# Kernel optimization log

Hardware: AMD Instinct MI355X
Metric: run time of the kernel (lower is better)

Reference implementation:

```python
import jax, jax.numpy as jnp
import numpy as np

N_V = 250        # n_vertices (hardcoded in module)
NUM_WS = 14
W_DIM = 512
Z_DIM = 512
B = 64
E_PER = 1488     # ~directed convex-hull edges per graph (3N-6 undirected)
LR = 0.01        # lr_multiplier
CAM_R = 1.3


def _fc(x, w, b):
    # StyleGAN FullyConnectedLayer: runtime weight gain lr/sqrt(fan_in), bias gain lr,
    # bias_act 'lrelu' (alpha=0.2) with gain sqrt(2).
    gain = LR / np.sqrt(w.shape[1])
    y = x @ (w.T * gain) + b * LR
    return jax.nn.leaky_relu(y, 0.2) * np.sqrt(2.0)


def _seg_mean(vals, idx, n):
    s = jax.ops.segment_sum(vals, idx, num_segments=n)
    c = jax.ops.segment_sum(jnp.ones((idx.shape[0], 1), vals.dtype), idx, num_segments=n)
    return s / jnp.maximum(c, 1.0)


def _processor(x, edge_index, edge_attr, ew0, eb0, ew1, eb1, nw0, nb0, nw1, nb1, out_dim):
    src, dst = edge_index[0], edge_index[1]
    # edge encoder on [x_recv, x_send, edge_attr]
    ef = jnp.concatenate([x[src], x[dst], edge_attr], axis=-1)
    ef = _fc(_fc(ef, ew0, eb0), ew1, eb1)
    # PyG propagate (flow source_to_target): message = cat([x_i, edge_attr]) with
    # x_i = x[edge_index[1]], mean-aggregated onto edge_index[1].
    msg = jnp.concatenate([x[dst], ef], axis=-1)
    agg = _seg_mean(msg, dst, x.shape[0])
    nf = jnp.concatenate([x, agg[:, out_dim:]], axis=-1)
    nf = _fc(_fc(nf, nw0, nb0), nw1, nb1)
    return nf, ef


def setup_inputs() -> dict:
    key = jax.random.key(0)
    ks = jax.random.split(key, 24)
    z = jax.random.normal(ks[0], (B, Z_DIM), jnp.float32)
    la = jax.random.normal(ks[1], (B * N_V, 3), jnp.float32)
    look_ats = -CAM_R * la / jnp.linalg.norm(la, axis=-1, keepdims=True)
    # block-structured edges: each graph's edges stay within its 250-node block
    rng = np.random.default_rng(0)
    base = np.repeat(np.arange(B, dtype=np.int32) * N_V, E_PER)
    src = base + rng.integers(0, N_V, size=B * E_PER).astype(np.int32)
    dst = base + rng.integers(0, N_V, size=B * E_PER).astype(np.int32)
    edge_index = jnp.asarray(np.stack([src, dst]))
    # FullyConnectedLayer weights: init N(0,1)/lr_multiplier, bias 0
    def w(k, o, i):
        return jax.random.normal(k, (o, i), jnp.float32) / LR
    D = W_DIM
    inp = dict(z=z, look_ats=look_ats, edge_index=edge_index)
    inp.update(
        p0_ew0=w(ks[2], D, 1034), p0_eb0=jnp.zeros((D,), jnp.float32),
        p0_ew1=w(ks[3], D, D),    p0_eb1=jnp.zeros((D,), jnp.float32),
        p0_nw0=w(ks[4], D, 1030), p0_nb0=jnp.zeros((D,), jnp.float32),
        p0_nw1=w(ks[5], D, D),    p0_nb1=jnp.zeros((D,), jnp.float32),
        p1_ew0=w(ks[6], D, 1536), p1_eb0=jnp.zeros((D,), jnp.float32),
        p1_ew1=w(ks[7], D, D),    p1_eb1=jnp.zeros((D,), jnp.float32),
        p1_nw0=w(ks[8], D, 1024), p1_nb0=jnp.zeros((D,), jnp.float32),
        p1_nw1=w(ks[9], D, D),    p1_nb1=jnp.zeros((D,), jnp.float32),
    )
    return inp


def reference(z, look_ats, edge_index,
              p0_ew0, p0_eb0, p0_ew1, p0_eb1, p0_nw0, p0_nb0, p0_nw1, p0_nb1,
              p1_ew0, p1_eb0, p1_ew1, p1_eb1, p1_nw0, p1_nb0, p1_nw1, p1_nb1):
    b = z.shape[0]
    # normalize_2nd_moment
    zn = z * jax.lax.rsqrt(jnp.mean(jnp.square(z), axis=-1, keepdims=True) + 1e-8)
    # generate_graph: x = cat([z.repeat(N,1), look_ats]); edge_attr from look_ats
    x = jnp.concatenate([jnp.tile(zn, (N_V, 1)), look_ats], axis=-1)  # [B*N, 515]
    rel = look_ats[edge_index[1]] - look_ats[edge_index[0]]
    dist = jnp.linalg.norm(rel, axis=-1, keepdims=True)
    ea = jnp.concatenate([rel, dist], axis=-1)  # [E, 4]
    x, ea = _processor(x, edge_index, ea, p0_ew0, p0_eb0, p0_ew1, p0_eb1,
                       p0_nw0, p0_nb0, p0_nw1, p0_nb1, W_DIM)
    x, ea = _processor(x, edge_index, ea, p1_ew0, p1_eb0, p1_ew1, p1_eb1,
                       p1_nw0, p1_nb0, p1_nw1, p1_nb1, W_DIM)
    ws = x[::N_V]                        # in_ids = [i*N for i in range(B)]
    return jnp.tile(ws[:, None, :], (1, NUM_WS, 1))  # [B, num_ws, w_dim]
```

## Files before the change

kernel.cpp:

```cpp
#include <hip/hip_runtime.h>
#include <hip/hip_bf16.h>
#include <cmath>

#define NVP 250
#define NN  16000
#define EN  95232
#define LRc 0.01f
#define SQ2 1.41421356237309515f

#define CAP_ES 1024
#define CAP_N1 1024
#define CAP_E0 4096
#define EBLK ((EN + 255) / 256)
#define NBLK ((NN + 255) / 256)
#define SK_T 4

typedef __attribute__((ext_vector_type(8))) short bf16x8;
typedef __attribute__((ext_vector_type(4))) float f32x4;

__device__ __forceinline__ unsigned short bfc(float x) {
  unsigned u = __builtin_bit_cast(unsigned, x);
  u = (u + 0x7fffu + ((u >> 16) & 1u)) >> 16;
  return (unsigned short)u;
}
__device__ __forceinline__ unsigned pk2(float a, float b) {
  return (unsigned)bfc(a) | ((unsigned)bfc(b) << 16);
}

struct GMX {
  const float* W; const float* Ain; float* pbuf; const int* Mdev;
  const float* cnt; const int* listN1;
  int Wld, Woff, Astride, K, KC, Mcap, Mfix;
};

template<int VECW, int SCALED>
__global__ __launch_bounds__(256) void gemmM2(GMX p) {
  int M = p.Mdev ? *p.Mdev : p.Mfix;
  if (M > p.Mcap) M = p.Mcap;
  const int mBase = blockIdx.x * 64;
  if (mBase >= M) return;
  const int nBase = blockIdx.y * 64;
  const int z = blockIdx.z;
  int kBeg = z * p.KC, kEnd = kBeg + p.KC;
  if (kEnd > p.K) kEnd = p.K;

  __shared__ unsigned short Abf[64*72];
  __shared__ unsigned short Wbf[64*72];
  const int t = threadIdx.x;
  const int srow = t >> 2, sq = (t & 3) * 16;
  int arow = mBase + srow; if (arow >= M) arow = M - 1;
  float s = 1.f;
  if (SCALED) s = 1.0f / fmaxf(p.cnt[p.listN1[arow]], 1.0f);
  const float* aRow = p.Ain + (size_t)arow * p.Astride + sq;
  const float* wRow = p.W + (size_t)(nBase + srow) * p.Wld + p.Woff + sq;

  float4 ra[4], rw[4];
  auto ld = [&](int kt) {
#pragma unroll
    for (int i = 0; i < 4; i++) {
      ra[i] = *(const float4*)(aRow + kt + 4*i);
      if (VECW) {
        rw[i] = *(const float4*)(wRow + kt + 4*i);
      } else {
        const float* wp = wRow + kt + 4*i;
        rw[i] = make_float4(wp[0], wp[1], wp[2], wp[3]);
      }
    }
  };
  ld(kBeg);

  const int lane = t & 63, wv = t >> 6;
  const int fr = wv*16 + (lane & 15);
  const int fcol = (lane & 15);
  const int fo = (lane >> 4) * 8;
  f32x4 acc0 = {}, acc1 = {}, acc2 = {}, acc3 = {};

  for (int kt = kBeg; kt < kEnd; kt += 64) {
    if (kt > kBeg) __syncthreads();
    unsigned short* da = &Abf[srow*72 + sq];
    unsigned short* dw = &Wbf[srow*72 + sq];
#pragma unroll
    for (int i = 0; i < 4; i++) {
      uint2 ua; ua.x = pk2(ra[i].x*s, ra[i].y*s); ua.y = pk2(ra[i].z*s, ra[i].w*s);
      *(uint2*)&da[i*4] = ua;
      uint2 uw; uw.x = pk2(rw[i].x, rw[i].y); uw.y = pk2(rw[i].z, rw[i].w);
      *(uint2*)&dw[i*4] = uw;
    }
    __syncthreads();
    if (kt + 64 < kEnd) ld(kt + 64);
#pragma unroll
    for (int kk = 0; kk < 64; kk += 32) {
      bf16x8 a = *(const bf16x8*)&Abf[fr*72 + kk + fo];
      bf16x8 b0 = *(const bf16x8*)&Wbf[( 0 + fcol)*72 + kk + fo];
      bf16x8 b1 = *(const bf16x8*)&Wbf[(16 + fcol)*72 + kk + fo];
      bf16x8 b2 = *(const bf16x8*)&Wbf[(32 + fcol)*72 + kk + fo];
      bf16x8 b3 = *(const bf16x8*)&Wbf[(48 + fcol)*72 + kk + fo];
      acc0 = __builtin_amdgcn_mfma_f32_16x16x32_bf16(a, b0, acc0, 0, 0, 0);
      acc1 = __builtin_amdgcn_mfma_f32_16x16x32_bf16(a, b1, acc1, 0, 0, 0);
      acc2 = __builtin_amdgcn_mfma_f32_16x16x32_bf16(a, b2, acc2, 0, 0, 0);
      acc3 = __builtin_amdgcn_mfma_f32_16x16x32_bf16(a, b3, acc3, 0, 0, 0);
    }
  }
  float* ob = p.pbuf + (size_t)z * p.Mcap * 512;
  int orow = mBase + wv*16 + (lane >> 4) * 4;
  int oc = nBase + fcol;
#pragma unroll
  for (int r = 0; r < 4; r++) {
    float* q = ob + (size_t)(orow + r) * 512 + oc;
    q[0] = acc0[r]; q[16] = acc1[r]; q[32] = acc2[r]; q[48] = acc3[r];
  }
}

struct GMG {
  const float* W; const float* x1c; const float* ef0c;
  const int* listES; const int* src; const int* dst; const int* posN; const int* posOf;
  const int* Mdev; float* pbuf; int KC;
};
__global__ __launch_bounds__(256) void gemmGM2(GMG p) {
  int M = *p.Mdev; if (M > CAP_ES) M = CAP_ES;
  const int mBase = blockIdx.x * 64;
  if (mBase >= M) return;
  const int nBase = blockIdx.y * 64;
  const int z = blockIdx.z;
  int kBeg = z * p.KC, kEnd = kBeg + p.KC;

  __shared__ unsigned short Abf[64*72];
  __shared__ unsigned short Wbf[64*72];
  const int t = threadIdx.x;
  const int srow = t >> 2, sq = (t & 3) * 16;
  int arow = mBase + srow; if (arow >= M) arow = M - 1;
  int e = p.listES[arow];
  const float* s0 = p.x1c + (size_t)p.posN[p.src[e]] * 512;
  const float* s1 = p.x1c + (size_t)p.posN[p.dst[e]] * 512;
  const float* s2 = p.ef0c + (size_t)p.posOf[e] * 512;
  const float* wRow = p.W + (size_t)(nBase + srow) * 1536 + sq;

  float4 ra[4], rw[4];
  auto ld = [&](int kt) {
    int ka = kt + sq;
    const float* ap = (ka < 512) ? (s0 + ka) : (ka < 1024) ? (s1 + ka - 512)
                                                           : (s2 + ka - 1024);
#pragma unroll
    for (int i = 0; i < 4; i++) {
      ra[i] = *(const float4*)(ap + 4*i);
      rw[i] = *(const float4*)(wRow + kt + 4*i);
    }
  };
  ld(kBeg);

  const int lane = t & 63, wv = t >> 6;
  const int fr = wv*16 + (lane & 15);
  const int fcol = (lane & 15);
  const int fo = (lane >> 4) * 8;
  f32x4 acc0 = {}, acc1 = {}, acc2 = {}, acc3 = {};

  for (int kt = kBeg; kt < kEnd; kt += 64) {
    if (kt > kBeg) __syncthreads();
    unsigned short* da = &Abf[srow*72 + sq];
    unsigned short* dw = &Wbf[srow*72 + sq];
#pragma unroll
    for (int i = 0; i < 4; i++) {
      uint2 ua; ua.x = pk2(ra[i].x, ra[i].y); ua.y = pk2(ra[i].z, ra[i].w);
      *(uint2*)&da[i*4] = ua;
      uint2 uw; uw.x = pk2(rw[i].x, rw[i].y); uw.y = pk2(rw[i].z, rw[i].w);
      *(uint2*)&dw[i*4] = uw;
    }
    __syncthreads();
    if (kt + 64 < kEnd) ld(kt + 64);
#pragma unroll
    for (int kk = 0; kk < 64; kk += 32) {
      bf16x8 a = *(const bf16x8*)&Abf[fr*72 + kk + fo];
      bf16x8 b0 = *(const bf16x8*)&Wbf[( 0 + fcol)*72 + kk + fo];
      bf16x8 b1 = *(const bf16x8*)&Wbf[(16 + fcol)*72 + kk + fo];
      bf16x8 b2 = *(const bf16x8*)&Wbf[(32 + fcol)*72 + kk + fo];
      bf16x8 b3 = *(const bf16x8*)&Wbf[(48 + fcol)*72 + kk + fo];
      acc0 = __builtin_amdgcn_mfma_f32_16x16x32_bf16(a, b0, acc0, 0, 0, 0);
      acc1 = __builtin_amdgcn_mfma_f32_16x16x32_bf16(a, b1, acc1, 0, 0, 0);
      acc2 = __builtin_amdgcn_mfma_f32_16x16x32_bf16(a, b2, acc2, 0, 0, 0);
      acc3 = __builtin_amdgcn_mfma_f32_16x16x32_bf16(a, b3, acc3, 0, 0, 0);
    }
  }
  float* ob = p.pbuf + (size_t)z * CAP_ES * 512;
  int orow = mBase + wv*16 + (lane >> 4) * 4;
  int oc = nBase + fcol;
#pragma unroll
  for (int r = 0; r < 4; r++) {
    float* q = ob + (size_t)(orow + r) * 512 + oc;
    q[0] = acc0[r]; q[16] = acc1[r]; q[32] = acc2[r]; q[48] = acc3[r];
  }
}

template<int VECW, int NSEG>
__device__ __forceinline__ void gemm_loop(
    const float* const* b0, const float* const* b1,
    const float* sc0, const float* sc1,
    const float* w0, const float* w1, const float* w2, const float* w3,
    int kBeg, int kEnd,
    float (*As)[36], float (*Bs)[68], float acc[4][4]) {
  const int t = threadIdx.x;
  const int k4 = (t & 7) * 4;
  const int mr = t >> 3;
  const int tx = t & 15, ty = t >> 4;
  float4 ra0, ra1, rw0, rw1, rw2, rw3;
  auto lA = [&](int k0) {
// ... 33 lines not shown
    if (k0 + 32 < kEnd) { lA(k0 + 32); lW(k0 + 32); }
#pragma unroll
    for (int kk = 0; kk < 32; kk++) {
      float4 a4 = *(const float4*)&As[kk][ty*4];
      float4 b4 = *(const float4*)&Bs[kk][tx*4];
      float aa[4] = {a4.x, a4.y, a4.z, a4.w};
      float bb[4] = {b4.x, b4.y, b4.z, b4.w};
#pragma unroll
      for (int i = 0; i < 4; i++)
#pragma unroll
        for (int j = 0; j < 4; j++) acc[i][j] += aa[i]*bb[j];
    }
  }
}

struct GPP {
  const float* W; const float* Ain; float* pbuf; const int* Mdev;
  const float* cnt; const int* listN1;
  int Wld, Woff, Astride, K, KC, Mcap, Mfix;
};
template<int VECW, int SCALED>
__global__ __launch_bounds__(128) void gemmP(GPP p) {
  int M = p.Mdev ? *p.Mdev : p.Mfix;
  if (M > p.Mcap) M = p.Mcap;
  const int mBase = blockIdx.x * 32;
  if (mBase >= M) return;
  const int nBase = blockIdx.y * 64;
  const int z = blockIdx.z;
  int kBeg = z * p.KC;
  int kEnd = kBeg + p.KC; if (kEnd > p.K) kEnd = p.K;
  __shared__ float As[32][36];
  __shared__ float Bs[32][68];
  const int t = threadIdx.x;
  const float* b0[1]; const float* b1[1]; float sc0[1] = {1.f}, sc1[1] = {1.f};
  int rA = mBase + (t >> 3);
  b0[0] = p.Ain + (size_t)rA * p.Astride;
  b1[0] = b0[0] + (size_t)16 * p.Astride;
  if (SCALED) {
    int ra = rA < M ? rA : M-1;
    int rb = (rA+16) < M ? rA+16 : M-1;
    sc0[0] = 1.0f / fmaxf(p.cnt[p.listN1[ra]], 1.0f);
    sc1[0] = 1.0f / fmaxf(p.cnt[p.listN1[rb]], 1.0f);
  }
  const int kofs = (t & 7)*4 + p.Woff;
  const float* w0 = p.W + (size_t)(nBase + (t>>3)) * p.Wld + kofs;
  const float* w1 = w0 + (size_t)16 * p.Wld;
  const float* w2 = w0 + (size_t)32 * p.Wld;
  const float* w3 = w0 + (size_t)48 * p.Wld;
  float acc[4][4] = {};
  gemm_loop<VECW, 1>(b0, b1, sc0, sc1, w0, w1, w2, w3, kBeg, kEnd, As, Bs, acc);
  const int tx = t & 15, ty = t >> 4;
#pragma unroll
  for (int i = 0; i < 4; i++) {
    int r = mBase + ty*4 + i;
    *(float4*)&p.pbuf[((size_t)z*p.Mcap + r)*512 + nBase + tx*4] =
      make_float4(acc[i][0],acc[i][1],acc[i][2],acc[i][3]);
  }
}

struct GTP {
  const float* W; const float* x1c; const float* agg1c; const float* cnt;
  const int* posN; float* pbuf; int KC;
};
__global__ __launch_bounds__(128) void gemmT(GTP p) {
  const int mBase = blockIdx.x * 32;
  const int nBase = blockIdx.y * 64;
  const int z = blockIdx.z;
  int kBeg = z * p.KC, kEnd = kBeg + p.KC;
  __shared__ float As[32][36];
  __shared__ float Bs[32][68];
  const int t = threadIdx.x;
  int r0 = mBase + (t>>3), r1 = r0 + 16;
  const float* b0[2] = { p.x1c + (size_t)p.posN[r0*NVP]*512,
                         p.agg1c + (size_t)r0*512 - 512 };
  const float* b1[2] = { p.x1c + (size_t)p.posN[r1*NVP]*512,
                         p.agg1c + (size_t)r1*512 - 512 };
  float sc0[2] = {1.f, 1.0f / fmaxf(p.cnt[r0*NVP], 1.0f)};
  float sc1[2] = {1.f, 1.0f / fmaxf(p.cnt[r1*NVP], 1.0f)};
  const int kofs = (t & 7)*4;
  const float* w0 = p.W + (size_t)(nBase + (t>>3)) * 1024 + kofs;
  const float* w1 = w0 + (size_t)16 * 1024;
  const float* w2 = w0 + (size_t)32 * 1024;
  const float* w3 = w0 + (size_t)48 * 1024;
  float acc[4][4] = {};
  gemm_loop<1, 2>(b0, b1, sc0, sc1, w0, w1, w2, w3, kBeg, kEnd, As, Bs, acc);
  const int tx = t & 15, ty = t >> 4;
#pragma unroll
  for (int i = 0; i < 4; i++) {
    int r = mBase + ty*4 + i;
    *(float4*)&p.pbuf[((size_t)z*64 + r)*512 + nBase + tx*4] =
      make_float4(acc[i][0],acc[i][1],acc[i][2],acc[i][3]);
  }
}

struct TABP { const float* zn; const float* We; const float* Wn;
              float* pbTs; float* pbTd; float* pbT0; };
__global__ __launch_bounds__(128) void tab_k(TABP q) {
  int wsel = blockIdx.y >> 3;
  int nBase = (blockIdx.y & 7) * 64;
  const float* W = (wsel == 2) ? q.Wn : q.We;
  int Wld = (wsel == 2) ? 1030 : 1034;
  int Woff = (wsel == 1) ? 515 : 0;
  float* pb = (wsel == 0) ? q.pbTs : (wsel == 1) ? q.pbTd : q.pbT0;
  int z = blockIdx.z;
  __shared__ float As[32][36];
  __shared__ float Bs[32][68];
// ... 6 lines not shown
  const float* w0 = W + (size_t)(nBase + (t>>3)) * Wld + kofs;
  const float* w1 = w0 + (size_t)16 * Wld;
  const float* w2 = w0 + (size_t)32 * Wld;
  const float* w3 = w0 + (size_t)48 * Wld;
  float acc[4][4] = {};
  gemm_loop<0, 1>(b0, b1, sc0, sc1, w0, w1, w2, w3, z*128, z*128+128, As, Bs, acc);
  const int tx = t & 15, ty = t >> 4;
#pragma unroll
  for (int i = 0; i < 4; i++) {
    int r = mBase + ty*4 + i;
    *(float4*)&pb[((size_t)z*64 + r)*512 + nBase + tx*4] =
      make_float4(acc[i][0],acc[i][1],acc[i][2],acc[i][3]);
  }
}

struct EPP {
  const float* pbuf; const float* bias; const float* T0p; const float* la;
  const float* cnt; const float* w0n;
  const int* rmap; const int* dst; const int* posN; const int* Mdev;
  float* outp; float* atomp;
  int SK, Mcap, Mfix; float gain;
};

template<int EPI>
__global__ __launch_bounds__(256) void epi_k(EPP e) {
  int M = e.Mdev ? *e.Mdev : e.Mfix;
  if (M > e.Mcap) M = e.Mcap;
  int i = blockIdx.x*256 + threadIdx.x;
  if (i >= M*128) return;
  int m = i >> 7, n4 = (i & 127) * 4;
  float ys[4] = {0.f, 0.f, 0.f, 0.f};
  for (int z = 0; z < e.SK; z++) {
    float4 v = *(const float4*)&e.pbuf[((size_t)z*e.Mcap + m)*512 + n4];
    ys[0] += v.x; ys[1] += v.y; ys[2] += v.z; ys[3] += v.w;
  }
  if (EPI == 7) {
    int nd = e.rmap[m];
    int rr = nd & 63;
#pragma unroll
    for (int z = 0; z < SK_T; z++) {
      float4 v = *(const float4*)&e.T0p[((size_t)z*64 + rr)*512 + n4];
      ys[0] += v.x; ys[1] += v.y; ys[2] += v.z; ys[3] += v.w;
    }
    float l0 = e.la[nd*3], l1 = e.la[nd*3+1], l2 = e.la[nd*3+2];
    bool has = e.cnt[nd] > 0.f;
#pragma unroll
    for (int j = 0; j < 4; j++) {
      int n = n4 + j;
      float corr = l0*e.w0n[0*512+n] + l1*e.w0n[1*512+n] + l2*e.w0n[2*512+n];
      if (has) corr += l0*e.w0n[3*512+n] + l1*e.w0n[4*512+n] + l2*e.w0n[5*512+n];
      ys[j] += corr;
    }
  }
#pragma unroll
  for (int j = 0; j < 4; j++) {
    float y = ys[j] * e.gain + e.bias[n4+j] * LRc;
    ys[j] = (y > 0.f ? y : 0.2f*y) * SQ2;
  }
  float4 ov = make_float4(ys[0], ys[1], ys[2], ys[3]);
  if (EPI == 0 || EPI == 7) {
    *(float4*)&e.outp[(size_t)m*512 + n4] = ov;
  } else if (EPI == 1) {
    *(float4*)&e.outp[(size_t)m*512 + n4] = ov;
    int tr = e.posN[e.dst[e.rmap[m]]];
#pragma unroll
    for (int j = 0; j < 4; j++) atomicAdd(&e.atomp[(size_t)tr*512 + n4 + j], ys[j]);
  } else if (EPI == 2) {
    int tr = e.dst[e.rmap[m]] / NVP;
#pragma unroll
    for (int j = 0; j < 4; j++) atomicAdd(&e.atomp[(size_t)tr*512 + n4 + j], ys[j]);
  } else {
#pragma unroll
    for (int w = 0; w < 14; w++)
      *(float4*)&e.outp[((size_t)(m*14 + w))*512 + n4] = ov;
  }
}

__global__ __launch_bounds__(256) void init_k(const float* z, float* zn, int* need,
                                              const float* W0, const float* Wn,
                                              float* w0s, float* w0n) {
  int b = blockIdx.x, t = threadIdx.x;
  if (b < 64) {
    float s = 0.f;
    for (int j = t; j < 512; j += 256) { float v = z[b*512+j]; s += v*v; }
    for (int o = 32; o > 0; o >>= 1) s += __shfl_down(s, o);
    __shared__ float red[5];
    if ((t & 63) == 0) red[t >> 6] = s;
    __syncthreads();
    if (t == 0) {
      float tot = red[0]+red[1]+red[2]+red[3];
      red[4] = 1.0f / sqrtf(tot * (1.0f/512.0f) + 1e-8f);
    }
// ... 20 lines not shown
  unsigned long long m = __ballot(pred);
  int lane = threadIdx.x & 63, w = threadIdx.x >> 6;
  if (lane == 0) ws4[w] = __popcll(m);
  __syncthreads();
  return ws4[0] + ws4[1] + ws4[2] + ws4[3];
}
__device__ __forceinline__ int blockRank(int pred, int* ws4) {
  unsigned long long m = __ballot(pred);
  int lane = threadIdx.x & 63, w = threadIdx.x >> 6;
  if (lane == 0) ws4[w] = __popcll(m);
  __syncthreads();
  int off = 0;
  for (int i = 0; i < w; i++) off += ws4[i];
  return off + __popcll(m & ((1ull << lane) - 1ull));
}

__global__ __launch_bounds__(256) void cntES_k(const int* src, const int* dst,
                                               float* cnt, int* need, int* bcnt) {
  __shared__ int ws4[4];
  int e = blockIdx.x*256 + threadIdx.x;
  int pred = 0;
  if (e < EN) {
    int d = dst[e];
    atomicAdd(&cnt[d], 1.0f);
    pred = (d % NVP) == 0;
    if (pred) need[src[e]] = 1;
  }
  int c = blockCount(pred, ws4);
  if (threadIdx.x == 0) bcnt[blockIdx.x] = c;
}
// ... 1 lines not shown
                                                 int* bcntE, int* bcntN) {
  __shared__ int ws4[4];
  int b = blockIdx.x;
  if (b < EBLK) {
    int e = b*256 + threadIdx.x;
    int pred = (e < EN) && need[dst[e]];
    int c = blockCount(pred, ws4);
    if (threadIdx.x == 0) bcntE[b] = c;
  } else {
    int n = (b-EBLK)*256 + threadIdx.x;
    int pred = (n < NN) && need[n];
    int c = blockCount(pred, ws4);
    if (threadIdx.x == 0) bcntN[b-EBLK] = c;
  }
}
__global__ __launch_bounds__(512) void scan3_k(const int* bA, int nA, int* oA, int* tA,
                                               const int* bB, int nB, int* oB, int* tB,
                                               const int* bC, int nC, int* oC, int* tC) {
  const int* bcnt; int n; int* boff; int* tot;
  if (blockIdx.x == 0)      { bcnt = bA; n = nA; boff = oA; tot = tA; }
  else if (blockIdx.x == 1) { bcnt = bB; n = nB; boff = oB; tot = tB; }
  else                      { bcnt = bC; n = nC; boff = oC; tot = tC; }
  __shared__ int s[512];
  int t = threadIdx.x;
  int orig = (t < n) ? bcnt[t] : 0;
  s[t] = orig;
  __syncthreads();
  for (int o = 1; o < 512; o <<= 1) {
    int v = (t >= o) ? s[t-o] : 0;
    __syncthreads();
    s[t] += v;
    __syncthreads();
  }
  if (t < n) boff[t] = s[t] - orig;
  if (t == n-1) *tot = s[t];
}
__global__ __launch_bounds__(256) void emit3_k(const int* src, const int* dst,
                                               const int* need,
                                               const int* boffS, int* listES,
                                               const int* boffE, int* listE0, int* posOf,
                                               const int* boffN, int* listN1, int* posN) {
  __shared__ int ws4[4];
  int b = blockIdx.x;
  if (b < EBLK) {
    int e = b*256 + threadIdx.x;
    int pred = (e < EN) && (dst[e] % NVP == 0);
    int rank = blockRank(pred, ws4);
    if (pred) {
      int pos = boffS[b] + rank;
      if (pos < CAP_ES) listES[pos] = e;
    }
  } else if (b < 2*EBLK) {
    int e = (b-EBLK)*256 + threadIdx.x;
    int pred = (e < EN) && need[dst[e]];
    int rank = blockRank(pred, ws4);
    if (pred) {
      int pos = boffE[b-EBLK] + rank;
      if (pos < CAP_E0) { listE0[pos] = e; posOf[e] = pos; }
    }
  } else {
    int n = (b-2*EBLK)*256 + threadIdx.x;
    int pred = (n < NN) && need[n];
    int rank = blockRank(pred, ws4);
    if (pred) {
      int pos = boffN[b-2*EBLK] + rank;
      if (pos < CAP_N1) { listN1[pos] = n; posN[n] = pos; }
    }
  }
}

__global__ __launch_bounds__(128) void edge0_k(const int* nE0p, const int* listE0,
                                               const int* src, const int* dst,
                                               const float* pbTs, const float* pbTd,
                                               const float* la, const float* w0s,
                                               const float* b0, float* h0c) {
  int i = blockIdx.x;
  int n0 = *nE0p; if (n0 > CAP_E0) n0 = CAP_E0;
  if (i >= n0) return;
  int tid = threadIdx.x;
  int e = listE0[i];
  int s = src[e], d = dst[e];
  float a0 = la[s*3], a1 = la[s*3+1], a2 = la[s*3+2];
// ... 47 lines not shown
  const float* p1eb1 = (const float*)d_in[14];
  const float* p1nw0 = (const float*)d_in[15];
  const float* p1nb0 = (const float*)d_in[16];
  const float* p1nw1 = (const float*)d_in[17];
  const float* p1nb1 = (const float*)d_in[18];
  const int* src = ei;
  const int* dst = ei + EN;

  char* ws = (char*)d_ws;
  size_t off = 0;
  auto al = [&](size_t bytes) -> void* {
    void* r = (void*)(ws + off);
    off += (bytes + 255) & ~(size_t)255;
    return r;
  };
  int*   tot    = (int*)  al(3*4);
  float* cnt    = (float*)al(NN*4);
  int*   need   = (int*)  al(NN*4);
  int*   posN   = (int*)  al(NN*4);
  int*   posOf  = (int*)  al((size_t)EN*4);
  int*   bcntS  = (int*)  al(EBLK*4);
  int*   boffS  = (int*)  al(EBLK*4);
  int*   bcntE  = (int*)  al(EBLK*4);
  int*   boffE  = (int*)  al(EBLK*4);
  int*   bcntN  = (int*)  al(NBLK*4);
  int*   boffN  = (int*)  al(NBLK*4);
  int*   listES = (int*)  al(CAP_ES*4);
  int*   listN1 = (int*)  al(CAP_N1*4);
  int*   listE0 = (int*)  al(CAP_E0*4);
  float* agg0c  = (float*)al((size_t)CAP_N1*512*4);
  float* agg1c  = (float*)al(64*512*4);
  size_t zEnd = off;
  float* zn     = (float*)al(64*512*4);
  float* w0s    = (float*)al(10*512*4);
  float* w0n    = (float*)al(6*512*4);
  float* pbTs   = (float*)al((size_t)SK_T*64*512*4);
  float* pbTd   = (float*)al((size_t)SK_T*64*512*4);
  float* pbT0   = (float*)al((size_t)SK_T*64*512*4);
  float* h0c    = (float*)al((size_t)CAP_E0*512*4);
  float* ef0c   = (float*)al((size_t)CAP_E0*512*4);
  float* hn1    = (float*)al((size_t)CAP_N1*512*4);
  float* x1c    = (float*)al((size_t)CAP_N1*512*4);
  float* hs     = (float*)al((size_t)CAP_ES*512*4);
  float* hn64   = (float*)al(64*512*4);
  float* pbuf   = (float*)al((size_t)16384*512*4);

  hipMemsetAsync(ws, 0, zEnd, stream);

  init_k<<<129, 256, 0, stream>>>(z, zn, need, p0ew0, p0nw0, w0s, w0n);
  cntES_k<<<EBLK, 256, 0, stream>>>(src, dst, cnt, need, bcntS);
  cntE0N1_k<<<EBLK+NBLK, 256, 0, stream>>>(dst, need, bcntE, bcntN);
  scan3_k<<<3, 512, 0, stream>>>(bcntS, EBLK, boffS, tot+0,
                                 bcntE, EBLK, boffE, tot+1,
                                 bcntN, NBLK, boffN, tot+2);
  emit3_k<<<2*EBLK+NBLK, 256, 0, stream>>>(src, dst, need, boffS, listES,
                                           boffE, listE0, posOf, boffN, listN1, posN);
  {
    TABP q{zn, p0ew0, p0nw0, pbTs, pbTd, pbT0};
    tab_k<<<dim3(2, 24, SK_T), 128, 0, stream>>>(q);
  }
  edge0_k<<<CAP_E0, 128, 0, stream>>>(tot+1, listE0, src, dst, pbTs, pbTd, la, w0s,
                                      p0eb0, h0c);

  {
    GMX p{}; p.W = p0ew1; p.Wld = 512; p.Woff = 0; p.Astride = 512;
    p.K = 512; p.KC = 256; p.Mcap = CAP_E0; p.Mdev = tot+1; p.Ain = h0c; p.pbuf = pbuf;
    gemmM2<1,0><<<dim3(CAP_E0/64, 8, 2), 256, 0, stream>>>(p);
    EPP e{}; e.pbuf = pbuf; e.SK = 2; e.Mcap = CAP_E0; e.Mdev = tot+1;
    e.bias = p0eb1; e.gain = LRc/sqrtf(512.f);
    e.rmap = listE0; e.dst = dst; e.posN = posN; e.outp = ef0c; e.atomp = agg0c;
    epi_k<1><<<(CAP_E0*128)/256, 256, 0, stream>>>(e);
  }
  {
    GMX p{}; p.W = p0nw0; p.Wld = 1030; p.Woff = 518; p.Astride = 512;
    p.K = 512; p.KC = 128; p.Mcap = CAP_N1; p.Mdev = tot+2;
    p.Ain = agg0c; p.cnt = cnt; p.listN1 = listN1; p.pbuf = pbuf;
    gemmM2<0,1><<<dim3(CAP_N1/64, 8, 4), 256, 0, stream>>>(p);
    EPP e{}; e.pbuf = pbuf; e.SK = 4; e.Mcap = CAP_N1; e.Mdev = tot+2;
    e.bias = p0nb0; e.gain = LRc/sqrtf(1030.f);
    e.T0p = pbT0; e.rmap = listN1; e.la = la; e.cnt = cnt; e.w0n = w0n; e.outp = hn1;
    epi_k<7><<<(CAP_N1*128)/256, 256, 0, stream>>>(e);
  }
  {
    GMX p{}; p.W = p0nw1; p.Wld = 512; p.Woff = 0; p.Astride = 512;
    p.K = 512; p.KC = 128; p.Mcap = CAP_N1; p.Mdev = tot+2; p.Ain = hn1; p.pbuf = pbuf;
    gemmM2<1,0><<<dim3(CAP_N1/64, 8, 4), 256, 0, stream>>>(p);
    EPP e{}; e.pbuf = pbuf; e.SK = 4; e.Mcap = CAP_N1; e.Mdev = tot+2;
    e.bias = p0nb1; e.gain = LRc/sqrtf(512.f); e.outp = x1c;
    epi_k<0><<<(CAP_N1*128)/256, 256, 0, stream>>>(e);
  }
  {
    GMG p{}; p.W = p1ew0; p.x1c = x1c; p.ef0c = ef0c;
    p.listES = listES; p.src = src; p.dst = dst; p.posN = posN; p.posOf = posOf;
    p.Mdev = tot+0; p.pbuf = pbuf; p.KC = 256;
    gemmGM2<<<dim3(CAP_ES/64, 8, 6), 256, 0, stream>>>(p);
    EPP e{}; e.pbuf = pbuf; e.SK = 6; e.Mcap = CAP_ES; e.Mdev = tot+0;
    e.bias = p1eb0; e.gain = LRc/sqrtf(1536.f); e.outp = hs;
    epi_k<0><<<(CAP_ES*128)/256, 256, 0, stream>>>(e);
  }
  {
    GMX p{}; p.W = p1ew1; p.Wld = 512; p.Woff = 0; p.Astride = 512;
    p.K = 512; p.KC = 128; p.Mcap = CAP_ES; p.Mdev = tot+0; p.Ain = hs; p.pbuf = pbuf;
    gemmM2<1,0><<<dim3(CAP_ES/64, 8, 4), 256, 0, stream>>>(p);
    EPP e{}; e.pbuf = pbuf; e.SK = 4; e.Mcap = CAP_ES; e.Mdev = tot+0;
    e.bias = p1eb1; e.gain = LRc/sqrtf(512.f);
    e.rmap = listES; e.dst = dst; e.atomp = agg1c;
    epi_k<2><<<(CAP_ES*128)/256, 256, 0, stream>>>(e);
  }
  {
    GTP p{}; p.W = p1nw0; p.x1c = x1c; p.agg1c = agg1c; p.cnt = cnt;
    p.posN = posN; p.pbuf = pbuf; p.KC = 128;
    gemmT<<<dim3(2, 8, 8), 128, 0, stream>>>(p);
    EPP e{}; e.pbuf = pbuf; e.SK = 8; e.Mcap = 64; e.Mfix = 64;
    e.bias = p1nb0; e.gain = LRc/sqrtf(1024.f); e.outp = hn64;
    epi_k<0><<<(64*128)/256, 256, 0, stream>>>(e);
  }
  {
    GPP p{}; p.W = p1nw1; p.Wld = 512; p.Woff = 0; p.Astride = 512;
    p.K = 512; p.KC = 128; p.Mcap = 64; p.Mfix = 64; p.Mdev = nullptr;
    p.Ain = hn64; p.pbuf = pbuf;
    gemmP<1,0><<<dim3(2, 8, 4), 128, 0, stream>>>(p);
    EPP e{}; e.pbuf = pbuf; e.SK = 4; e.Mcap = 64; e.Mfix = 64;
    e.bias = p1nb1; e.gain = LRc/sqrtf(512.f); e.outp = (float*)d_out;
    epi_k<8><<<(64*128)/256, 256, 0, stream>>>(e);
  }
}
```

Before: 145.5 us.

## Fuse GEMM epilogues into kernels, drop split-K, merge scan into emit

Removes split-K partial buffers and the separate epilogue kernels. Each GEMM now runs the full K loop and applies bias, leaky-relu, row remapping and scatter atomics straight from the MFMA accumulators. The scan kernel is also folded into the emit kernel, where each block recomputes its prefix by summing the block counts. This cuts about seven kernel launches and the partial-sum traffic, but each kernel now has fewer blocks with longer K loops, and epilogue stores and atomics become less coalesced.

```diff
diff --git a/kernel.cpp b/kernel.cpp
--- a/kernel.cpp
+++ b/kernel.cpp
@@ -27,22 +27,85 @@
   return (unsigned)bfc(a) | ((unsigned)bfc(b) << 16);
 }
 
-struct GMX {
-  const float* W; const float* Ain; float* pbuf; const int* Mdev;
+struct FEP {
+  const float* bias; float gain;
+  const float* T0p; const float* la; const float* cnt; const float* w0n;
+  const int* rmap; const int* dst; const int* posN;
+  float* outp; float* atomp;
+};
+
+template<int EPI>
+__device__ __forceinline__ void mfma_epi(const FEP& f, f32x4 acc0, f32x4 acc1,
+                                         f32x4 acc2, f32x4 acc3,
+                                         int mBase, int nBase, int M,
+                                         int lane, int wv) {
+  const int fcol = lane & 15;
+  int rows[4]; bool rok[4]; int tr[4];
+  int rr4[4]; float la0[4], la1[4], la2[4]; bool has[4];
+#pragma unroll
+  for (int r = 0; r < 4; r++) {
+    int row = mBase + wv*16 + (lane >> 4)*4 + r;
+    rows[r] = row; rok[r] = row < M;
+    int rc = rok[r] ? row : 0;
+    if (EPI == 1) tr[r] = f.posN[f.dst[f.rmap[rc]]];
+    if (EPI == 2) tr[r] = f.dst[f.rmap[rc]] / NVP;
+    if (EPI == 7) {
+      int nd = f.rmap[rc];
+      rr4[r] = nd & 63;
+      la0[r] = f.la[nd*3]; la1[r] = f.la[nd*3+1]; la2[r] = f.la[nd*3+2];
+      has[r] = f.cnt[nd] > 0.f;
+    }
+  }
+  f32x4 accs[4] = {acc0, acc1, acc2, acc3};
+#pragma unroll
+  for (int c = 0; c < 4; c++) {
+    int n = nBase + fcol + 16*c;
+    float bi = f.bias[n] * LRc;
+    float w6[6];
+    if (EPI == 7) {
+#pragma unroll
+      for (int j = 0; j < 6; j++) w6[j] = f.w0n[j*512 + n];
+    }
+#pragma unroll
+    for (int r = 0; r < 4; r++) {
+      if (!rok[r]) continue;
+      float yr = accs[c][r];
+      if (EPI == 7) {
+#pragma unroll
+        for (int zz = 0; zz < SK_T; zz++)
+          yr += f.T0p[((size_t)zz*64 + rr4[r])*512 + n];
+        float corr = la0[r]*w6[0] + la1[r]*w6[1] + la2[r]*w6[2];
+        if (has[r]) corr += la0[r]*w6[3] + la1[r]*w6[4] + la2[r]*w6[5];
+        yr += corr;
+      }
+      float y = yr * f.gain + bi;
+      y = (y > 0.f ? y : 0.2f*y) * SQ2;
+      if (EPI == 0 || EPI == 7) {
+        f.outp[(size_t)rows[r]*512 + n] = y;
+      } else if (EPI == 1) {
+        f.outp[(size_t)rows[r]*512 + n] = y;
+        atomicAdd(&f.atomp[(size_t)tr[r]*512 + n], y);
+      } else {
+        atomicAdd(&f.atomp[(size_t)tr[r]*512 + n], y);
+      }
+    }
+  }
+}
+
+struct GMF {
+  const float* W; const float* Ain; const int* Mdev;
   const float* cnt; const int* listN1;
-  int Wld, Woff, Astride, K, KC, Mcap, Mfix;
+  int Wld, Woff, Astride, K, Mcap, Mfix;
+  FEP f;
 };
 
-template<int VECW, int SCALED>
-__global__ __launch_bounds__(256) void gemmM2(GMX p) {
+template<int VECW, int SCALED, int EPI>
+__global__ __launch_bounds__(256) void gemmMF(GMF p) {
   int M = p.Mdev ? *p.Mdev : p.Mfix;
   if (M > p.Mcap) M = p.Mcap;
   const int mBase = blockIdx.x * 64;
   if (mBase >= M) return;
   const int nBase = blockIdx.y * 64;
-  const int z = blockIdx.z;
-  int kBeg = z * p.KC, kEnd = kBeg + p.KC;
-  if (kEnd > p.K) kEnd = p.K;
 
   __shared__ unsigned short Abf[64*72];
   __shared__ unsigned short Wbf[64*72];
@@ -67,7 +130,7 @@
       }
     }
   };
-  ld(kBeg);
+  ld(0);
 
   const int lane = t & 63, wv = t >> 6;
   const int fr = wv*16 + (lane & 15);
@@ -75,8 +138,8 @@
   const int fo = (lane >> 4) * 8;
   f32x4 acc0 = {}, acc1 = {}, acc2 = {}, acc3 = {};
 
-  for (int kt = kBeg; kt < kEnd; kt += 64) {
-    if (kt > kBeg) __syncthreads();
+  for (int kt = 0; kt < p.K; kt += 64) {
+    if (kt > 0) __syncthreads();
     unsigned short* da = &Abf[srow*72 + sq];
     unsigned short* dw = &Wbf[srow*72 + sq];
 #pragma unroll
@@ -87,7 +150,7 @@
       *(uint2*)&dw[i*4] = uw;
     }
     __syncthreads();
-    if (kt + 64 < kEnd) ld(kt + 64);
+    if (kt + 64 < p.K) ld(kt + 64);
 #pragma unroll
     for (int kk = 0; kk < 64; kk += 32) {
       bf16x8 a = *(const bf16x8*)&Abf[fr*72 + kk + fo];
@@ -101,28 +164,20 @@
       acc3 = __builtin_amdgcn_mfma_f32_16x16x32_bf16(a, b3, acc3, 0, 0, 0);
     }
   }
-  float* ob = p.pbuf + (size_t)z * p.Mcap * 512;
-  int orow = mBase + wv*16 + (lane >> 4) * 4;
-  int oc = nBase + fcol;
-#pragma unroll
-  for (int r = 0; r < 4; r++) {
-    float* q = ob + (size_t)(orow + r) * 512 + oc;
-    q[0] = acc0[r]; q[16] = acc1[r]; q[32] = acc2[r]; q[48] = acc3[r];
-  }
-}
-
-struct GMG {
+  mfma_epi<EPI>(p.f, acc0, acc1, acc2, acc3, mBase, nBase, M, lane, wv);
+}
+
+struct GGF {
   const float* W; const float* x1c; const float* ef0c;
   const int* listES; const int* src; const int* dst; const int* posN; const int* posOf;
-  const int* Mdev; float* pbuf; int KC;
+  const int* Mdev;
+  FEP f;
 };
-__global__ __launch_bounds__(256) void gemmGM2(GMG p) {
+__global__ __launch_bounds__(256) void gemmGF(GGF p) {
   int M = *p.Mdev; if (M > CAP_ES) M = CAP_ES;
   const int mBase = blockIdx.x * 64;
   if (mBase >= M) return;
   const int nBase = blockIdx.y * 64;
-  const int z = blockIdx.z;
-  int kBeg = z * p.KC, kEnd = kBeg + p.KC;
 
   __shared__ unsigned short Abf[64*72];
   __shared__ unsigned short Wbf[64*72];
@@ -146,7 +201,7 @@
       rw[i] = *(const float4*)(wRow + kt + 4*i);
     }
   };
-  ld(kBeg);
+  ld(0);
 
   const int lane = t & 63, wv = t >> 6;
   const int fr = wv*16 + (lane & 15);
@@ -154,8 +209,8 @@
   const int fo = (lane >> 4) * 8;
   f32x4 acc0 = {}, acc1 = {}, acc2 = {}, acc3 = {};
 
-  for (int kt = kBeg; kt < kEnd; kt += 64) {
-    if (kt > kBeg) __syncthreads();
+  for (int kt = 0; kt < 1536; kt += 64) {
+    if (kt > 0) __syncthreads();
     unsigned short* da = &Abf[srow*72 + sq];
     unsigned short* dw = &Wbf[srow*72 + sq];
 #pragma unroll
@@ -166,7 +221,7 @@
       *(uint2*)&dw[i*4] = uw;
     }
     __syncthreads();
-    if (kt + 64 < kEnd) ld(kt + 64);
+    if (kt + 64 < 1536) ld(kt + 64);
 #pragma unroll
     for (int kk = 0; kk < 64; kk += 32) {
       bf16x8 a = *(const bf16x8*)&Abf[fr*72 + kk + fo];
@@ -180,14 +235,7 @@
       acc3 = __builtin_amdgcn_mfma_f32_16x16x32_bf16(a, b3, acc3, 0, 0, 0);
     }
   }
-  float* ob = p.pbuf + (size_t)z * CAP_ES * 512;
-  int orow = mBase + wv*16 + (lane >> 4) * 4;
-  int oc = nBase + fcol;
-#pragma unroll
-  for (int r = 0; r < 4; r++) {
-    float* q = ob + (size_t)(orow + r) * 512 + oc;
-    q[0] = acc0[r]; q[16] = acc1[r]; q[32] = acc2[r]; q[48] = acc3[r];
-  }
+  mfma_epi<0>(p.f, acc0, acc1, acc2, acc3, mBase, nBase, M, lane, wv);
 }
 
 template<int VECW, int NSEG>
@@ -251,59 +299,14 @@
   }
 }
 
-struct GPP {
-  const float* W; const float* Ain; float* pbuf; const int* Mdev;
-  const float* cnt; const int* listN1;
-  int Wld, Woff, Astride, K, KC, Mcap, Mfix;
+struct GTF {
+  const float* W; const float* x1c; const float* agg1c; const float* cnt;
+  const int* posN;
+  const float* bias; float gain; float* outp;
 };
-template<int VECW, int SCALED>
-__global__ __launch_bounds__(128) void gemmP(GPP p) {
-  int M = p.Mdev ? *p.Mdev : p.Mfix;
-  if (M > p.Mcap) M = p.Mcap;
-  const int mBase = blockIdx.x * 32;
-  if (mBase >= M) return;
-  const int nBase = blockIdx.y * 64;
-  const int z = blockIdx.z;
-  int kBeg = z * p.KC;
-  int kEnd = kBeg + p.KC; if (kEnd > p.K) kEnd = p.K;
-  __shared__ float As[32][36];
-  __shared__ float Bs[32][68];
-  const int t = threadIdx.x;
-  const float* b0[1]; const float* b1[1]; float sc0[1] = {1.f}, sc1[1] = {1.f};
-  int rA = mBase + (t >> 3);
-  b0[0] = p.Ain + (size_t)rA * p.Astride;
-  b1[0] = b0[0] + (size_t)16 * p.Astride;
-  if (SCALED) {
-    int ra = rA < M ? rA : M-1;
-    int rb = (rA+16) < M ? rA+16 : M-1;
-    sc0[0] = 1.0f / fmaxf(p.cnt[p.listN1[ra]], 1.0f);
-    sc1[0] = 1.0f / fmaxf(p.cnt[p.listN1[rb]], 1.0f);
-  }
-  const int kofs = (t & 7)*4 + p.Woff;
-  const float* w0 = p.W + (size_t)(nBase + (t>>3)) * p.Wld + kofs;
-  const float* w1 = w0 + (size_t)16 * p.Wld;
-  const float* w2 = w0 + (size_t)32 * p.Wld;
-  const float* w3 = w0 + (size_t)48 * p.Wld;
-  float acc[4][4] = {};
-  gemm_loop<VECW, 1>(b0, b1, sc0, sc1, w0, w1, w2, w3, kBeg, kEnd, As, Bs, acc);
-  const int tx = t & 15, ty = t >> 4;
-#pragma unroll
-  for (int i = 0; i < 4; i++) {
-    int r = mBase + ty*4 + i;
-    *(float4*)&p.pbuf[((size_t)z*p.Mcap + r)*512 + nBase + tx*4] =
-      make_float4(acc[i][0],acc[i][1],acc[i][2],acc[i][3]);
-  }
-}
-
-struct GTP {
-  const float* W; const float* x1c; const float* agg1c; const float* cnt;
-  const int* posN; float* pbuf; int KC;
-};
-__global__ __launch_bounds__(128) void gemmT(GTP p) {
+__global__ __launch_bounds__(128) void gemmTF(GTF p) {
   const int mBase = blockIdx.x * 32;
   const int nBase = blockIdx.y * 64;
-  const int z = blockIdx.z;
-  int kBeg = z * p.KC, kEnd = kBeg + p.KC;
   __shared__ float As[32][36];
   __shared__ float Bs[32][68];
   const int t = threadIdx.x;
@@ -320,13 +323,60 @@
   const float* w2 = w0 + (size_t)32 * 1024;
   const float* w3 = w0 + (size_t)48 * 1024;
   float acc[4][4] = {};
-  gemm_loop<1, 2>(b0, b1, sc0, sc1, w0, w1, w2, w3, kBeg, kEnd, As, Bs, acc);
+  gemm_loop<1, 2>(b0, b1, sc0, sc1, w0, w1, w2, w3, 0, 1024, As, Bs, acc);
   const int tx = t & 15, ty = t >> 4;
+  float4 bv = *(const float4*)&p.bias[nBase + tx*4];
+  float bb[4] = {bv.x, bv.y, bv.z, bv.w};
 #pragma unroll
   for (int i = 0; i < 4; i++) {
     int r = mBase + ty*4 + i;
-    *(float4*)&p.pbuf[((size_t)z*64 + r)*512 + nBase + tx*4] =
-      make_float4(acc[i][0],acc[i][1],acc[i][2],acc[i][3]);
+    float ys[4];
+#pragma unroll
+    for (int j = 0; j < 4; j++) {
+      float y = acc[i][j] * p.gain + bb[j] * LRc;
+      ys[j] = (y > 0.f ? y : 0.2f*y) * SQ2;
+    }
+    *(float4*)&p.outp[(size_t)r*512 + nBase + tx*4] =
+      make_float4(ys[0], ys[1], ys[2], ys[3]);
+  }
+}
+
+struct GPF2 {
+  const float* W; const float* Ain;
+  const float* bias; float gain; float* outp;
+};
+__global__ __launch_bounds__(128) void gemmPF(GPF2 p) {
+  const int mBase = blockIdx.x * 32;
+  const int nBase = blockIdx.y * 64;
+  __shared__ float As[32][36];
+  __shared__ float Bs[32][68];
+  const int t = threadIdx.x;
+  const float* b0[1]; const float* b1[1]; float sc0[1] = {1.f}, sc1[1] = {1.f};
+  b0[0] = p.Ain + (size_t)(mBase + (t>>3)) * 512;
+  b1[0] = b0[0] + (size_t)16 * 512;
+  const int kofs = (t & 7)*4;
+  const float* w0 = p.W + (size_t)(nBase + (t>>3)) * 512 + kofs;
+  const float* w1 = w0 + (size_t)16 * 512;
+  const float* w2 = w0 + (size_t)32 * 512;
+  const float* w3 = w0 + (size_t)48 * 512;
+  float acc[4][4] = {};
+  gemm_loop<1, 1>(b0, b1, sc0, sc1, w0, w1, w2, w3, 0, 512, As, Bs, acc);
+  const int tx = t & 15, ty = t >> 4;
+  float4 bv = *(const float4*)&p.bias[nBase + tx*4];
+  float bb[4] = {bv.x, bv.y, bv.z, bv.w};
+#pragma unroll
+  for (int i = 0; i < 4; i++) {
+    int r = mBase + ty*4 + i;
+    float ys[4];
+#pragma unroll
+    for (int j = 0; j < 4; j++) {
+      float y = acc[i][j] * p.gain + bb[j] * LRc;
+      ys[j] = (y > 0.f ? y : 0.2f*y) * SQ2;
+    }
+    float4 ov = make_float4(ys[0], ys[1], ys[2], ys[3]);
+#pragma unroll
+    for (int w = 0; w < 14; w++)
+      *(float4*)&p.outp[((size_t)(r*14 + w))*512 + nBase + tx*4] = ov;
   }
 }
 
@@ -363,68 +413,6 @@
   }
 }
 
-struct EPP {
-  const float* pbuf; const float* bias; const float* T0p; const float* la;
-  const float* cnt; const float* w0n;
-  const int* rmap; const int* dst; const int* posN; const int* Mdev;
-  float* outp; float* atomp;
-  int SK, Mcap, Mfix; float gain;
-};
-
-template<int EPI>
-__global__ __launch_bounds__(256) void epi_k(EPP e) {
-  int M = e.Mdev ? *e.Mdev : e.Mfix;
-  if (M > e.Mcap) M = e.Mcap;
-  int i = blockIdx.x*256 + threadIdx.x;
-  if (i >= M*128) return;
-  int m = i >> 7, n4 = (i & 127) * 4;
-  float ys[4] = {0.f, 0.f, 0.f, 0.f};
-  for (int z = 0; z < e.SK; z++) {
-    float4 v = *(const float4*)&e.pbuf[((size_t)z*e.Mcap + m)*512 + n4];
-    ys[0] += v.x; ys[1] += v.y; ys[2] += v.z; ys[3] += v.w;
-  }
-  if (EPI == 7) {
-    int nd = e.rmap[m];
-    int rr = nd & 63;
-#pragma unroll
-    for (int z = 0; z < SK_T; z++) {
-      float4 v = *(const float4*)&e.T0p[((size_t)z*64 + rr)*512 + n4];
-      ys[0] += v.x; ys[1] += v.y; ys[2] += v.z; ys[3] += v.w;
-    }
-    float l0 = e.la[nd*3], l1 = e.la[nd*3+1], l2 = e.la[nd*3+2];
-    bool has = e.cnt[nd] > 0.f;
-#pragma unroll
-    for (int j = 0; j < 4; j++) {
-      int n = n4 + j;
-      float corr = l0*e.w0n[0*512+n] + l1*e.w0n[1*512+n] + l2*e.w0n[2*512+n];
-      if (has) corr += l0*e.w0n[3*512+n] + l1*e.w0n[4*512+n] + l2*e.w0n[5*512+n];
-      ys[j] += corr;
-    }
-  }
-#pragma unroll
-  for (int j = 0; j < 4; j++) {
-    float y = ys[j] * e.gain + e.bias[n4+j] * LRc;
-    ys[j] = (y > 0.f ? y : 0.2f*y) * SQ2;
-  }
-  float4 ov = make_float4(ys[0], ys[1], ys[2], ys[3]);
-  if (EPI == 0 || EPI == 7) {
-    *(float4*)&e.outp[(size_t)m*512 + n4] = ov;
-  } else if (EPI == 1) {
-    *(float4*)&e.outp[(size_t)m*512 + n4] = ov;
-    int tr = e.posN[e.dst[e.rmap[m]]];
-#pragma unroll
-    for (int j = 0; j < 4; j++) atomicAdd(&e.atomp[(size_t)tr*512 + n4 + j], ys[j]);
-  } else if (EPI == 2) {
-    int tr = e.dst[e.rmap[m]] / NVP;
-#pragma unroll
-    for (int j = 0; j < 4; j++) atomicAdd(&e.atomp[(size_t)tr*512 + n4 + j], ys[j]);
-  } else {
-#pragma unroll
-    for (int w = 0; w < 14; w++)
-      *(float4*)&e.outp[((size_t)(m*14 + w))*512 + n4] = ov;
-  }
-}
-
 __global__ __launch_bounds__(256) void init_k(const float* z, float* zn, int* need,
                                               const float* W0, const float* Wn,
                                               float* w0s, float* w0n) {
@@ -475,6 +463,16 @@
   for (int i = 0; i < w; i++) off += ws4[i];
   return off + __popcll(m & ((1ull << lane) - 1ull));
 }
+__device__ __forceinline__ int blockSumN(const int* arr, int n, int* red) {
+  int local = 0;
+  for (int i = threadIdx.x; i < n; i += 256) local += arr[i];
+  for (int o = 32; o > 0; o >>= 1) local += __shfl_down(local, o);
+  if ((threadIdx.x & 63) == 0) red[threadIdx.x >> 6] = local;
+  __syncthreads();
+  int s = red[0]+red[1]+red[2]+red[3];
+  __syncthreads();
+  return s;
+}
 
 __global__ __launch_bounds__(256) void cntES_k(const int* src, const int* dst,
                                                float* cnt, int* need, int* bcnt) {
@@ -506,58 +504,41 @@
     if (threadIdx.x == 0) bcntN[b-EBLK] = c;
   }
 }
-__global__ __launch_bounds__(512) void scan3_k(const int* bA, int nA, int* oA, int* tA,
-                                               const int* bB, int nB, int* oB, int* tB,
-                                               const int* bC, int nC, int* oC, int* tC) {
-  const int* bcnt; int n; int* boff; int* tot;
-  if (blockIdx.x == 0)      { bcnt = bA; n = nA; boff = oA; tot = tA; }
-  else if (blockIdx.x == 1) { bcnt = bB; n = nB; boff = oB; tot = tB; }
-  else                      { bcnt = bC; n = nC; boff = oC; tot = tC; }
-  __shared__ int s[512];
-  int t = threadIdx.x;
-  int orig = (t < n) ? bcnt[t] : 0;
-  s[t] = orig;
-  __syncthreads();
-  for (int o = 1; o < 512; o <<= 1) {
-    int v = (t >= o) ? s[t-o] : 0;
-    __syncthreads();
-    s[t] += v;
-    __syncthreads();
-  }
-  if (t < n) boff[t] = s[t] - orig;
-  if (t == n-1) *tot = s[t];
-}
-__global__ __launch_bounds__(256) void emit3_k(const int* src, const int* dst,
-                                               const int* need,
-                                               const int* boffS, int* listES,
-                                               const int* boffE, int* listE0, int* posOf,
-                                               const int* boffN, int* listN1, int* posN) {
+__global__ __launch_bounds__(256) void emit3s_k(const int* src, const int* dst,
+                                                const int* need,
+                                                const int* bcntS, int* listES,
+                                                const int* bcntE, int* listE0, int* posOf,
+                                                const int* bcntN, int* listN1, int* posN,
+                                                int* tot) {
+  __shared__ int red[4];
   __shared__ int ws4[4];
   int b = blockIdx.x;
-  if (b < EBLK) {
-    int e = b*256 + threadIdx.x;
+  const int* bcnt; int bl, nblk, seg;
+  if (b < EBLK)        { seg = 0; bl = b;          bcnt = bcntS; nblk = EBLK; }
+  else if (b < 2*EBLK) { seg = 1; bl = b - EBLK;   bcnt = bcntE; nblk = EBLK; }
+  else                 { seg = 2; bl = b - 2*EBLK; bcnt = bcntN; nblk = NBLK; }
+  int boff = blockSumN(bcnt, bl, red);
+  if (bl == 0) {
+    int tt = blockSumN(bcnt, nblk, red);
+    if (threadIdx.x == 0) tot[seg] = tt;
+  }
+  if (seg == 0) {
+    int e = bl*256 + threadIdx.x;
     int pred = (e < EN) && (dst[e] % NVP == 0);
     int rank = blockRank(pred, ws4);
-    if (pred) {
-      int pos = boffS[b] + rank;
-      if (pos < CAP_ES) listES[pos] = e;
-    }
-  } else if (b < 2*EBLK) {
-    int e = (b-EBLK)*256 + threadIdx.x;
+    if (pred) { int pos = boff + rank; if (pos < CAP_ES) listES[pos] = e; }
+  } else if (seg == 1) {
+    int e = bl*256 + threadIdx.x;
     int pred = (e < EN) && need[dst[e]];
     int rank = blockRank(pred, ws4);
-    if (pred) {
-      int pos = boffE[b-EBLK] + rank;
-      if (pos < CAP_E0) { listE0[pos] = e; posOf[e] = pos; }
-    }
+    if (pred) { int pos = boff + rank;
+      if (pos < CAP_E0) { listE0[pos] = e; posOf[e] = pos; } }
   } else {
-    int n = (b-2*EBLK)*256 + threadIdx.x;
+    int n = bl*256 + threadIdx.x;
     int pred = (n < NN) && need[n];
     int rank = blockRank(pred, ws4);
-    if (pred) {
-      int pos = boffN[b-2*EBLK] + rank;
-      if (pos < CAP_N1) { listN1[pos] = n; posN[n] = pos; }
-    }
+    if (pred) { int pos = boff + rank;
+      if (pos < CAP_N1) { listN1[pos] = n; posN[n] = pos; } }
   }
 }
 
@@ -635,23 +616,20 @@
     off += (bytes + 255) & ~(size_t)255;
     return r;
   };
+  float* cnt    = (float*)al(NN*4);
+  float* agg0c  = (float*)al((size_t)CAP_N1*512*4);
+  float* agg1c  = (float*)al(64*512*4);
+  size_t zEnd = off;
   int*   tot    = (int*)  al(3*4);
-  float* cnt    = (float*)al(NN*4);
   int*   need   = (int*)  al(NN*4);
   int*   posN   = (int*)  al(NN*4);
   int*   posOf  = (int*)  al((size_t)EN*4);
   int*   bcntS  = (int*)  al(EBLK*4);
-  int*   boffS  = (int*)  al(EBLK*4);
   int*   bcntE  = (int*)  al(EBLK*4);
-  int*   boffE  = (int*)  al(EBLK*4);
   int*   bcntN  = (int*)  al(NBLK*4);
-  int*   boffN  = (int*)  al(NBLK*4);
   int*   listES = (int*)  al(CAP_ES*4);
   int*   listN1 = (int*)  al(CAP_N1*4);
   int*   listE0 = (int*)  al(CAP_E0*4);
-  float* agg0c  = (float*)al((size_t)CAP_N1*512*4);
-  float* agg1c  = (float*)al(64*512*4);
-  size_t zEnd = off;
   float* zn     = (float*)al(64*512*4);
   float* w0s    = (float*)al(10*512*4);
   float* w0n    = (float*)al(6*512*4);
@@ -664,18 +642,15 @@
   float* x1c    = (float*)al((size_t)CAP_N1*512*4);
   float* hs     = (float*)al((size_t)CAP_ES*512*4);
   float* hn64   = (float*)al(64*512*4);
-  float* pbuf   = (float*)al((size_t)16384*512*4);
 
   hipMemsetAsync(ws, 0, zEnd, stream);
 
   init_k<<<129, 256, 0, stream>>>(z, zn, need, p0ew0, p0nw0, w0s, w0n);
   cntES_k<<<EBLK, 256, 0, stream>>>(src, dst, cnt, need, bcntS);
   cntE0N1_k<<<EBLK+NBLK, 256, 0, stream>>>(dst, need, bcntE, bcntN);
-  scan3_k<<<3, 512, 0, stream>>>(bcntS, EBLK, boffS, tot+0,
-                                 bcntE, EBLK, boffE, tot+1,
-                                 bcntN, NBLK, boffN, tot+2);
-  emit3_k<<<2*EBLK+NBLK, 256, 0, stream>>>(src, dst, need, boffS, listES,
-                                           boffE, listE0, posOf, boffN, listN1, posN);
+  emit3s_k<<<2*EBLK+NBLK, 256, 0, stream>>>(src, dst, need, bcntS, listES,
+                                            bcntE, listE0, posOf,
+                                            bcntN, listN1, posN, tot);
   {
     TABP q{zn, p0ew0, p0nw0, pbTs, pbTd, pbT0};
     tab_k<<<dim3(2, 24, SK_T), 128, 0, stream>>>(q);
@@ -684,65 +659,50 @@
                                       p0eb0, h0c);
 
   {
-    GMX p{}; p.W = p0ew1; p.Wld = 512; p.Woff = 0; p.Astride = 512;
-    p.K = 512; p.KC = 256; p.Mcap = CAP_E0; p.Mdev = tot+1; p.Ain = h0c; p.pbuf = pbuf;
-    gemmM2<1,0><<<dim3(CAP_E0/64, 8, 2), 256, 0, stream>>>(p);
-    EPP e{}; e.pbuf = pbuf; e.SK = 2; e.Mcap = CAP_E0; e.Mdev = tot+1;
-    e.bias = p0eb1; e.gain = LRc/sqrtf(512.f);
-    e.rmap = listE0; e.dst = dst; e.posN = posN; e.outp = ef0c; e.atomp = agg0c;
-    epi_k<1><<<(CAP_E0*128)/256, 256, 0, stream>>>(e);
+    GMF p{}; p.W = p0ew1; p.Wld = 512; p.Woff = 0; p.Astride = 512;
+    p.K = 512; p.Mcap = CAP_E0; p.Mdev = tot+1; p.Ain = h0c;
+    p.f.bias = p0eb1; p.f.gain = LRc/sqrtf(512.f);
+    p.f.rmap = listE0; p.f.dst = dst; p.f.posN = posN;
+    p.f.outp = ef0c; p.f.atomp = agg0c;
+    gemmMF<1,0,1><<<dim3(CAP_E0/64, 8), 256, 0, stream>>>(p);
   }
   {
-    GMX p{}; p.W = p0nw0; p.Wld = 1030; p.Woff = 518; p.Astride = 512;
-    p.K = 512; p.KC = 128; p.Mcap = CAP_N1; p.Mdev = tot+2;
-    p.Ain = agg0c; p.cnt = cnt; p.listN1 = listN1; p.pbuf = pbuf;
-    gemmM2<0,1><<<dim3(CAP_N1/64, 8, 4), 256, 0, stream>>>(p);
-    EPP e{}; e.pbuf = pbuf; e.SK = 4; e.Mcap = CAP_N1; e.Mdev = tot+2;
-    e.bias = p0nb0; e.gain = LRc/sqrtf(1030.f);
-    e.T0p = pbT0; e.rmap = listN1; e.la = la; e.cnt = cnt; e.w0n = w0n; e.outp = hn1;
-    epi_k<7><<<(CAP_N1*128)/256, 256, 0, stream>>>(e);
+    GMF p{}; p.W = p0nw0; p.Wld = 1030; p.Woff = 518; p.Astride = 512;
+    p.K = 512; p.Mcap = CAP_N1; p.Mdev = tot+2;
+    p.Ain = agg0c; p.cnt = cnt; p.listN1 = listN1;
+    p.f.bias = p0nb0; p.f.gain = LRc/sqrtf(1030.f);
+    p.f.T0p = pbT0; p.f.la = la; p.f.cnt = cnt; p.f.w0n = w0n; p.f.rmap = listN1;
+    p.f.outp = hn1;
+    gemmMF<0,1,7><<<dim3(CAP_N1/64, 8), 256, 0, stream>>>(p);
   }
   {
-    GMX p{}; p.W = p0nw1; p.Wld = 512; p.Woff = 0; p.Astride = 512;
-    p.K = 512; p.KC = 128; p.Mcap = CAP_N1; p.Mdev = tot+2; p.Ain = hn1; p.pbuf = pbuf;
-    gemmM2<1,0><<<dim3(CAP_N1/64, 8, 4), 256, 0, stream>>>(p);
-    EPP e{}; e.pbuf = pbuf; e.SK = 4; e.Mcap = CAP_N1; e.Mdev = tot+2;
-    e.bias = p0nb1; e.gain = LRc/sqrtf(512.f); e.outp = x1c;
-    epi_k<0><<<(CAP_N1*128)/256, 256, 0, stream>>>(e);
+    GMF p{}; p.W = p0nw1; p.Wld = 512; p.Woff = 0; p.Astride = 512;
+    p.K = 512; p.Mcap = CAP_N1; p.Mdev = tot+2; p.Ain = hn1;
+    p.f.bias = p0nb1; p.f.gain = LRc/sqrtf(512.f); p.f.outp = x1c;
+    gemmMF<1,0,0><<<dim3(CAP_N1/64, 8), 256, 0, stream>>>(p);
   }
   {
-    GMG p{}; p.W = p1ew0; p.x1c = x1c; p.ef0c = ef0c;
+    GGF p{}; p.W = p1ew0; p.x1c = x1c; p.ef0c = ef0c;
     p.listES = listES; p.src = src; p.dst = dst; p.posN = posN; p.posOf = posOf;
-    p.Mdev = tot+0; p.pbuf = pbuf; p.KC = 256;
-    gemmGM2<<<dim3(CAP_ES/64, 8, 6), 256, 0, stream>>>(p);
-    EPP e{}; e.pbuf = pbuf; e.SK = 6; e.Mcap = CAP_ES; e.Mdev = tot+0;
-    e.bias = p1eb0; e.gain = LRc/sqrtf(1536.f); e.outp = hs;
-    epi_k<0><<<(CAP_ES*128)/256, 256, 0, stream>>>(e);
+    p.Mdev = tot+0;
+    p.f.bias = p1eb0; p.f.gain = LRc/sqrtf(1536.f); p.f.outp = hs;
+    gemmGF<<<dim3(CAP_ES/64, 8), 256, 0, stream>>>(p);
   }
   {
-    GMX p{}; p.W = p1ew1; p.Wld = 512; p.Woff = 0; p.Astride = 512;
-    p.K = 512; p.KC = 128; p.Mcap = CAP_ES; p.Mdev = tot+0; p.Ain = hs; p.pbuf = pbuf;
-    gemmM2<1,0><<<dim3(CAP_ES/64, 8, 4), 256, 0, stream>>>(p);
-    EPP e{}; e.pbuf = pbuf; e.SK = 4; e.Mcap = CAP_ES; e.Mdev = tot+0;
-    e.bias = p1eb1; e.gain = LRc/sqrtf(512.f);
-    e.rmap = listES; e.dst = dst; e.atomp = agg1c;
-    epi_k<2><<<(CAP_ES*128)/256, 256, 0, stream>>>(e);
+    GMF p{}; p.W = p1ew1; p.Wld = 512; p.Woff = 0; p.Astride = 512;
+    p.K = 512; p.Mcap = CAP_ES; p.Mdev = tot+0; p.Ain = hs;
+    p.f.bias = p1eb1; p.f.gain = LRc/sqrtf(512.f);
+    p.f.rmap = listES; p.f.dst = dst; p.f.atomp = agg1c;
+    gemmMF<1,0,2><<<dim3(CAP_ES/64, 8), 256, 0, stream>>>(p);
   }
   {
-    GTP p{}; p.W = p1nw0; p.x1c = x1c; p.agg1c = agg1c; p.cnt = cnt;
-    p.posN = posN; p.pbuf = pbuf; p.KC = 128;
-    gemmT<<<dim3(2, 8, 8), 128, 0, stream>>>(p);
-    EPP e{}; e.pbuf = pbuf; e.SK = 8; e.Mcap = 64; e.Mfix = 64;
-    e.bias = p1nb0; e.gain = LRc/sqrtf(1024.f); e.outp = hn64;
-    epi_k<0><<<(64*128)/256, 256, 0, stream>>>(e);
+    GTF p{}; p.W = p1nw0; p.x1c = x1c; p.agg1c = agg1c; p.cnt = cnt; p.posN = posN;
+    p.bias = p1nb0; p.gain = LRc/sqrtf(1024.f); p.outp = hn64;
+    gemmTF<<<dim3(2, 8), 128, 0, stream>>>(p);
   }
   {
-    GPP p{}; p.W = p1nw1; p.Wld = 512; p.Woff = 0; p.Astride = 512;
-    p.K = 512; p.KC = 128; p.Mcap = 64; p.Mfix = 64; p.Mdev = nullptr;
-    p.Ain = hn64; p.pbuf = pbuf;
-    gemmP<1,0><<<dim3(2, 8, 4), 128, 0, stream>>>(p);
-    EPP e{}; e.pbuf = pbuf; e.SK = 4; e.Mcap = 64; e.Mfix = 64;
-    e.bias = p1nb1; e.gain = LRc/sqrtf(512.f); e.outp = (float*)d_out;
-    epi_k<8><<<(64*128)/256, 256, 0, stream>>>(e);
-  }
-}
+    GPF2 p{}; p.W = p1nw1; p.Ain = hn64;
+    p.bias = p1nb1; p.gain = LRc/sqrtf(512.f); p.outp = (float*)d_out;
+    gemmPF<<<dim3(2, 8), 128, 0, stream>>>(p);
+  }
+}
```

Measured after the change: 201.1 us. 38.2% more time.
